# Optimization experiments

Measured on AMD Instinct MI355X. Metric: run time of the kernel, lower is better.

The kernel has to match this reference:

```python
import jax, jax.numpy as jnp
import numpy as np
from itertools import combinations

# ---- G(3,0,1) projective geometric algebra tables (blade order: grades 0..4, lexicographic) ----

def _build_tables():
    blades = [c for g in range(5) for c in combinations(range(4), g)]
    index = {b: i for i, b in enumerate(blades)}
    def mul(a, b, e0_sq):
        lst = list(a) + list(b)
        sign = 1
        for i in range(len(lst)):
            for j in range(len(lst) - 1 - i):
                if lst[j] > lst[j + 1]:
                    lst[j], lst[j + 1] = lst[j + 1], lst[j]
                    sign = -sign
        out, i = [], 0
        while i < len(lst):
            if i + 1 < len(lst) and lst[i] == lst[i + 1]:
                if lst[i] == 0:
                    sign *= e0_sq  # e0^2 = 0 in PGA geometric product
                i += 2
            else:
                out.append(lst[i]); i += 1
        return tuple(out), sign
    GP = np.zeros((16, 16, 16), np.float32)
    WEDGE = np.zeros((16, 16, 16), np.float32)
    for a in blades:
        for b in blades:
            bl, s = mul(a, b, 0)
            if s != 0:
                GP[index[a], index[b], index[bl]] += s
            if not (set(a) & set(b)):
                bl, s = mul(a, b, 1)
                WEDGE[index[a], index[b], index[bl]] += s
    D = np.zeros((16, 16), np.float32)
    for a in blades:
        c = tuple(sorted(set(range(4)) - set(a)))
        bl, s = mul(a, c, 1)  # e_a ^ e_c = s * e0123
        D[index[c], index[a]] = s
    Dinv = np.linalg.inv(D).astype(np.float32)
    # 9 Pin(3,0,1)-equivariant linear basis maps: 5 grade projections + 4 left-mult by e0
    B = np.zeros((9, 16, 16), np.float32)
    for i, a in enumerate(blades):
        B[len(a), i, i] = 1.0
        if 0 not in a:
            tgt = tuple(sorted((0,) + a))
            B[5 + len(a), index[tgt], i] = 1.0
    inner_idx = np.array([i for i, a in enumerate(blades) if 0 not in a])  # invariant inner product skips e0 blades
    return (jnp.asarray(GP), jnp.asarray(WEDGE), jnp.asarray(D), jnp.asarray(Dinv), jnp.asarray(B), jnp.asarray(inner_idx))

GP_T, WEDGE_T, DUAL, DUAL_INV, BASIS, INNER_IDX = _build_tables()
N_HEADS = 8  # gatr SelfAttentionConfig default


def equi_linear(x, W):
    # x: [..., in_ch, 16], W: [out_ch, in_ch, 9] -> [..., out_ch, 16]
    return jnp.einsum('...ik,oib,bjk->...oj', x, W, BASIS)


def equi_norm(x, eps=1e-6):
    sq = jnp.sum(jnp.take(x, INNER_IDX, axis=-1) ** 2, axis=-1)      # [..., C]
    factor = jnp.mean(sq, axis=-1, keepdims=True)[..., None]          # [..., 1, 1]
    return x * jax.lax.rsqrt(factor + eps)


def geometric_product(x, y):
    return jnp.einsum('...i,...j,ijk->...k', x, y, GP_T)


def equi_join(x, y):
    xd = jnp.einsum('ji,...i->...j', DUAL, x)
    yd = jnp.einsum('ji,...i->...j', DUAL, y)
    w = jnp.einsum('...i,...j,ijk->...k', xd, yd, WEDGE_T)
    return jnp.einsum('ji,...i->...j', DUAL_INV, w)


def attention(x, Wq, Wk, Wv, Wo):
    Bb, N, C, _ = x.shape
    ch = C // N_HEADS
    def split(h):
        return h.reshape(Bb, N, N_HEADS, ch, 16).transpose(0, 2, 1, 3, 4)  # [B,H,N,ch,16]
    q = split(equi_linear(x, Wq))
    k = split(equi_linear(x, Wk))
    v = split(equi_linear(x, Wv))
    qi = jnp.take(q, INNER_IDX, axis=-1)
    ki = jnp.take(k, INNER_IDX, axis=-1)
    logits = jnp.einsum('bhnck,bhmck->bhnm', qi, ki) / np.float32(np.sqrt(8 * ch))
    att = jax.nn.softmax(logits, axis=-1)
    out = jnp.einsum('bhnm,bhmck->bhnck', att, v)
    out = out.transpose(0, 2, 1, 3, 4).reshape(Bb, N, C, 16)
    return equi_linear(out, Wo)


def geo_mlp(x, Wl, Wr, Wm):
    C = x.shape[-2]
    half = C // 2
    left = equi_linear(x, Wl)
    right = equi_linear(x, Wr)
    gp = geometric_product(left[..., :half, :], right[..., :half, :])
    jn = equi_join(left[..., half:, :], right[..., half:, :])
    h = jnp.concatenate([gp, jn], axis=-2)
    h = h * jax.nn.gelu(h[..., 0:1], approximate=False)  # scalar-gated GELU
    return equi_linear(h, Wm)


def embed_point(p):
    # PGA point: homogeneous trivector, e123 coefficient 1
    z = jnp.zeros(p.shape[:-1] + (16,), p.dtype)
    z = z.at[..., 11].set(p[..., 2])
    z = z.at[..., 12].set(-p[..., 1])
    z = z.at[..., 13].set(p[..., 0])
    z = z.at[..., 14].set(1.0)
    return z


def reference(points, W_in, Wq, Wk, Wv, Wo, Wl, Wr, Wm, W_out):
    x = embed_point(points)[..., None, :]   # [B, N, 1, 16]
    x = equi_linear(x, W_in)                # [B, N, C, 16]
    def block(xc, p):
        wq, wk, wv, wo, wl, wr, wm = p
        xc = xc + attention(equi_norm(xc), wq, wk, wv, wo)
        xc = xc + geo_mlp(equi_norm(xc), wl, wr, wm)
        return xc, None
    x, _ = jax.lax.scan(block, x, (Wq, Wk, Wv, Wo, Wl, Wr, Wm))
    out = equi_linear(x, W_out)             # [B, N, 1, 16]
    return jnp.mean(out[..., 0], axis=(1, 2))  # [B]


def setup_inputs():
    key = jax.random.key(0)
    ks = jax.random.split(key, 12)
    B, N, C, L = 1, 2048, 16, 10
    def w(k, o, i):
        return jax.random.normal(k, (o, i, 9), jnp.float32) / np.float32(np.sqrt(9.0 * i))
    def wl(k, o, i):
        return jax.random.normal(k, (L, o, i, 9), jnp.float32) / np.float32(np.sqrt(9.0 * i))
    return {
        'points': jax.random.normal(ks[0], (B, N, 3), jnp.float32),
        'W_in': w(ks[1], C, 1),
        'Wq': wl(ks[2], C, C), 'Wk': wl(ks[3], C, C), 'Wv': wl(ks[4], C, C),
        'Wo': wl(ks[5], C, C), 'Wl': wl(ks[6], C, C), 'Wr': wl(ks[7], C, C),
        'Wm': wl(ks[8], C, C), 'W_out': w(ks[9], 1, C),
    }
```

## Files before the change

kernel.cpp:

```cpp
#include <hip/hip_runtime.h>
#include <math.h>

#define NTOK 2048

typedef short short8v __attribute__((ext_vector_type(8)));
typedef short short4v __attribute__((ext_vector_type(4)));
typedef float f32x4 __attribute__((ext_vector_type(4)));

__device__ __forceinline__ unsigned short f2bf(float x){
  unsigned u = __float_as_uint(x);
  u += 0x7fff + ((u>>16)&1);
  return (unsigned short)(u>>16);
}

struct GEnt { unsigned char i, j, k; signed char s; };

constexpr int IDX2MASK[16] = {0,1,2,4,8,3,5,9,6,10,12,7,11,13,14,15};
constexpr int MASK2IDX[16] = {0,1,2,5,3,6,8,11,4,7,9,12,10,13,14,15};

constexpr int rsign(int a, int b){
  int cnt=0;
  for(int i=0;i<4;++i) if((b>>i)&1) for(int j=i+1;j<4;++j) if((a>>j)&1) cnt++;
  return (cnt&1)?-1:1;
}

struct GPTab { GEnt e[192]; };
constexpr GPTab make_gp(){
  GPTab t{}; int n=0;
  for(int ia=0; ia<16; ++ia) for(int ib=0; ib<16; ++ib){
    int a=IDX2MASK[ia], b=IDX2MASK[ib];
    if(a&b&1) continue;
    t.e[n].i=(unsigned char)ia; t.e[n].j=(unsigned char)ib;
    t.e[n].k=(unsigned char)MASK2IDX[a^b]; t.e[n].s=(signed char)rsign(a,b);
    ++n;
  }
  return t;
}
static constexpr GPTab GP_TAB = make_gp();

struct JTab { GEnt e[81]; };
constexpr JTab make_join(){
  JTab t{}; int n=0;
  for(int ia=0; ia<16; ++ia) for(int ib=0; ib<16; ++ib){
    int a=IDX2MASK[ia], b=IDX2MASK[ib];
    if((a|b)!=15) continue;
    int ca=(~a)&15, cb=(~b)&15, k=a&b, ck=(~k)&15;
    int s = rsign(a,ca)*rsign(b,cb)*rsign(ca,cb)*rsign(k,ck);
    t.e[n].i=(unsigned char)ia; t.e[n].j=(unsigned char)ib;
    t.e[n].k=(unsigned char)MASK2IDX[k]; t.e[n].s=(signed char)s;
    ++n;
  }
  return t;
}
static constexpr JTab J_TAB = make_join();

constexpr int INNER[8] = {0,2,3,4,8,9,10,14};

__device__ __forceinline__ void apply_gp(float* o, const float* a, const float* b){
#pragma unroll
  for(int n=0;n<192;++n){
    const float s = (float)GP_TAB.e[n].s;
    o[GP_TAB.e[n].k] = fmaf(s*a[GP_TAB.e[n].i], b[GP_TAB.e[n].j], o[GP_TAB.e[n].k]);
  }
}
__device__ __forceinline__ void apply_join(float* o, const float* a, const float* b){
#pragma unroll
  for(int n=0;n<81;++n){
    const float s = (float)J_TAB.e[n].s;
    o[J_TAB.e[n].k] = fmaf(s*a[J_TAB.e[n].i], b[J_TAB.e[n].j], o[J_TAB.e[n].k]);
  }
}

__device__ __forceinline__ void elin_row(float acc[16], const float* xin, const float* w0p){
#pragma unroll
  for(int j=0;j<16;++j) acc[j]=0.0f;
#pragma unroll
  for(int i=0;i<16;++i){
    const float* w = w0p + i*9;
    const float4* xp = (const float4*)(xin + i*16);
    float4 A=xp[0], B=xp[1], Cc=xp[2], D=xp[3];
    float w0=w[0],w1=w[1],w2=w[2],w3=w[3],w4=w[4],w5=w[5],w6=w[6],w7=w[7],w8=w[8];
    acc[0] = fmaf(w0, A.x,  acc[0]);
    acc[1] = fmaf(w1, A.y,  acc[1]);
    acc[2] = fmaf(w1, A.z,  acc[2]);
    acc[3] = fmaf(w1, A.w,  acc[3]);
    acc[4] = fmaf(w1, B.x,  acc[4]);
    acc[5] = fmaf(w2, B.y,  acc[5]);
    acc[6] = fmaf(w2, B.z,  acc[6]);
    acc[7] = fmaf(w2, B.w,  acc[7]);
    acc[8] = fmaf(w2, Cc.x, acc[8]);
    acc[9] = fmaf(w2, Cc.y, acc[9]);
    acc[10]= fmaf(w2, Cc.z, acc[10]);
    acc[11]= fmaf(w3, Cc.w, acc[11]);
    acc[12]= fmaf(w3, D.x,  acc[12]);
    acc[13]= fmaf(w3, D.y,  acc[13]);
    acc[14]= fmaf(w3, D.z,  acc[14]);
    acc[15]= fmaf(w4, D.w,  acc[15]);
    acc[1] = fmaf(w5, A.x,  acc[1]);
    acc[5] = fmaf(w6, A.z,  acc[5]);
    acc[6] = fmaf(w6, A.w,  acc[6]);
    acc[7] = fmaf(w6, B.x,  acc[7]);
    acc[11]= fmaf(w7, Cc.x, acc[11]);
    acc[12]= fmaf(w7, Cc.y, acc[12]);
    acc[13]= fmaf(w7, Cc.z, acc[13]);
    acc[15]= fmaf(w8, D.z,  acc[15]);
  }
}

__device__ __forceinline__ float gelu_exact(float x){
  return 0.5f*x*(1.0f+erff(x*0.70710678118654752f));
}

#define WPAD 145
#define TBS  264
#define TPB  8

template<int MODE>
__global__ __launch_bounds__(128) void token_kernel(
    const float* __restrict__ points, const float* __restrict__ Win,
    const float* __restrict__ Wo, const float* __restrict__ Wl,
    const float* __restrict__ Wr, const float* __restrict__ Wm,
    const float* __restrict__ Wq, const float* __restrict__ Wk,
    const float* __restrict__ Wv, const float* __restrict__ Wout,
    const float* __restrict__ ATT, float* __restrict__ X,
    unsigned short* __restrict__ Qg16, unsigned short* __restrict__ Kg16,
    unsigned short* __restrict__ VgT, float* __restrict__ toksum)
{
  __shared__ float wlds[6*16*WPAD];
  __shared__ float buf[TPB*TBS];
  __shared__ float sred[TPB*16];
  const int tid = threadIdx.x;
  const int t = tid>>4, o = tid&15;
  const int n = blockIdx.x*TPB + t;

  auto stage = [&](float* dst, const float* src){
#pragma unroll
    for(int r=0;r<18;++r){
      int k = tid + r*128;
      dst[(k/144)*WPAD + (k%144)] = src[k];
    }
  };
  if (MODE==0){ stage(wlds+3*16*WPAD, Wq); stage(wlds+4*16*WPAD, Wk); stage(wlds+5*16*WPAD, Wv); }
  if (MODE==1){ stage(wlds+0*16*WPAD, Wl); stage(wlds+1*16*WPAD, Wr); stage(wlds+2*16*WPAD, Wm);
                stage(wlds+3*16*WPAD, Wq); stage(wlds+4*16*WPAD, Wk); stage(wlds+5*16*WPAD, Wv); }
  if (MODE==2){ stage(wlds+0*16*WPAD, Wl); stage(wlds+1*16*WPAD, Wr); stage(wlds+2*16*WPAD, Wm); }

  float* tb = buf + t*TBS;
  float xr[16];

  if (MODE==0){
    float px = points[n*3+0], py = points[n*3+1], pz = points[n*3+2];
    float w3 = Win[o*9+3], w8 = Win[o*9+8];
#pragma unroll
    for(int j=0;j<16;++j) xr[j]=0.0f;
    xr[11]= w3*pz; xr[12]= -w3*py; xr[13]= w3*px; xr[14]= w3; xr[15]= w8;
    float4* xg = (float4*)(X + (size_t)n*256 + o*16);
    xg[0]=make_float4(xr[0],xr[1],xr[2],xr[3]);
    xg[1]=make_float4(xr[4],xr[5],xr[6],xr[7]);
    xg[2]=make_float4(xr[8],xr[9],xr[10],xr[11]);
    xg[3]=make_float4(xr[12],xr[13],xr[14],xr[15]);
  } else {
    const float4* xg = (const float4*)(X + (size_t)n*256 + o*16);
    float4 a=xg[0],b=xg[1],c=xg[2],d=xg[3];
    xr[0]=a.x; xr[1]=a.y; xr[2]=a.z; xr[3]=a.w;
    xr[4]=b.x; xr[5]=b.y; xr[6]=b.z; xr[7]=b.w;
    xr[8]=c.x; xr[9]=c.y; xr[10]=c.z; xr[11]=c.w;
    xr[12]=d.x; xr[13]=d.y; xr[14]=d.z; xr[15]=d.w;
    const float4* ag = (const float4*)(ATT + (size_t)n*256 + o*16);
    float4* bp = (float4*)(tb + o*16);
    bp[0]=ag[0]; bp[1]=ag[1]; bp[2]=ag[2]; bp[3]=ag[3];
    __syncthreads();
    float acc[16];
    elin_row(acc, tb, Wo + o*144);
#pragma unroll
    for(int j=0;j<16;++j) xr[j]+=acc[j];
    float s=0;
#pragma unroll
    for(int z=0;z<8;++z){ float v=xr[INNER[z]]; s=fmaf(v,v,s); }
    sred[tid]=s; __syncthreads();
    float tot=0;
#pragma unroll
    for(int c2=0;c2<16;++c2) tot += sred[t*16+c2];
    float f = 1.0f/sqrtf(tot*(1.0f/16.0f)+1e-6f);
    float4* bp2=(float4*)(tb+o*16);
    bp2[0]=make_float4(xr[0]*f,xr[1]*f,xr[2]*f,xr[3]*f);
    bp2[1]=make_float4(xr[4]*f,xr[5]*f,xr[6]*f,xr[7]*f);
    bp2[2]=make_float4(xr[8]*f,xr[9]*f,xr[10]*f,xr[11]*f);
    bp2[3]=make_float4(xr[12]*f,xr[13]*f,xr[14]*f,xr[15]*f);
    __syncthreads();
    float L[16], R[16];
    elin_row(L, tb, wlds+0*16*WPAD + o*WPAD);
    elin_row(R, tb, wlds+1*16*WPAD + o*WPAD);
    float h[16];
#pragma unroll
    for(int j=0;j<16;++j) h[j]=0.0f;
    if (o<8) apply_gp(h,L,R); else apply_join(h,L,R);
    float gel = gelu_exact(h[0]);
#pragma unroll
    for(int j=0;j<16;++j) h[j]*=gel;
    __syncthreads();
    float4* bp3=(float4*)(tb+o*16);
    bp3[0]=make_float4(h[0],h[1],h[2],h[3]);
    bp3[1]=make_float4(h[4],h[5],h[6],h[7]);
    bp3[2]=make_float4(h[8],h[9],h[10],h[11]);
    bp3[3]=make_float4(h[12],h[13],h[14],h[15]);
    __syncthreads();
    float mm2[16];
    elin_row(mm2, tb, wlds+2*16*WPAD + o*WPAD);
#pragma unroll
    for(int j=0;j<16;++j) xr[j]+=mm2[j];
    if (MODE==1){
      float4* xs = (float4*)(X + (size_t)n*256 + o*16);
      xs[0]=make_float4(xr[0],xr[1],xr[2],xr[3]);
      xs[1]=make_float4(xr[4],xr[5],xr[6],xr[7]);
      xs[2]=make_float4(xr[8],xr[9],xr[10],xr[11]);
      xs[3]=make_float4(xr[12],xr[13],xr[14],xr[15]);
    }
  }

  if (MODE==2){
    sred[tid] = Wout[o*9]*xr[0];
    __syncthreads();
    if (o==0){
      float s2=0;
#pragma unroll
      for(int c2=0;c2<16;++c2) s2+=sred[t*16+c2];
      toksum[n]=s2;
    }
    return;
  }

  {
    float s=0;
#pragma unroll
    for(int z=0;z<8;++z){ float v=xr[INNER[z]]; s=fmaf(v,v,s); }
    sred[tid]=s; __syncthreads();
    float tot=0;
#pragma unroll
    for(int c2=0;c2<16;++c2) tot += sred[t*16+c2];
    float f2 = 1.0f/sqrtf(tot*(1.0f/16.0f)+1e-6f);
    float4* bp4=(float4*)(tb+o*16);
    bp4[0]=make_float4(xr[0]*f2,xr[1]*f2,xr[2]*f2,xr[3]*f2);
    bp4[1]=make_float4(xr[4]*f2,xr[5]*f2,xr[6]*f2,xr[7]*f2);
    bp4[2]=make_float4(xr[8]*f2,xr[9]*f2,xr[10]*f2,xr[11]*f2);
    bp4[3]=make_float4(xr[12]*f2,xr[13]*f2,xr[14]*f2,xr[15]*f2);
    __syncthreads();
    float q_[16],k_[16],v_[16];
    elin_row(q_, tb, wlds+3*16*WPAD+o*WPAD);
    elin_row(k_, tb, wlds+4*16*WPAD+o*WPAD);
    elin_row(v_, tb, wlds+5*16*WPAD+o*WPAD);
    int hh=o>>1, cc=o&1;
    {
      unsigned qw[4], kw[4];
#pragma unroll
      for(int j=0;j<4;++j){
        unsigned short a0=f2bf(q_[INNER[2*j]]*0.25f), a1=f2bf(q_[INNER[2*j+1]]*0.25f);
        unsigned short b0=f2bf(k_[INNER[2*j]]),       b1=f2bf(k_[INNER[2*j+1]]);
        qw[j] = (unsigned)a0 | ((unsigned)a1<<16);
        kw[j] = (unsigned)b0 | ((unsigned)b1<<16);
      }
      size_t rb = ((size_t)hh*NTOK + n)*16 + cc*8;
      *(uint4*)(Qg16 + rb) = make_uint4(qw[0],qw[1],qw[2],qw[3]);
      *(uint4*)(Kg16 + rb) = make_uint4(kw[0],kw[1],kw[2],kw[3]);
    }
    __syncthreads();
    {
      float4* vb = (float4*)(tb + o*16);
      vb[0]=make_float4(v_[0],v_[1],v_[2],v_[3]);
      vb[1]=make_float4(v_[4],v_[5],v_[6],v_[7]);
      vb[2]=make_float4(v_[8],v_[9],v_[10],v_[11]);
      vb[3]=make_float4(v_[12],v_[13],v_[14],v_[15]);
    }
    __syncthreads();
#pragma unroll
    for(int pp=0;pp<2;++pp){
      int p  = tid + pp*128;
      int h2 = p>>5, v2 = p&31;
      int oc = 2*h2 + (v2>>4), c2 = v2&15;
      unsigned vw[4];
#pragma unroll
      for(int j=0;j<4;++j){
        unsigned short e0=f2bf(buf[(2*j  )*TBS + oc*16 + c2]);
        unsigned short e1=f2bf(buf[(2*j+1)*TBS + oc*16 + c2]);
        vw[j]=(unsigned)e0 | ((unsigned)e1<<16);
      }
      *(uint4*)(VgT + ((size_t)(h2*32+v2))*NTOK + (size_t)blockIdx.x*TPB) = make_uint4(vw[0],vw[1],vw[2],vw[3]);
    }
  }
}

__global__ __launch_bounds__(256) void attn_kernel(
    const unsigned short* __restrict__ Qg16, const unsigned short* __restrict__ Kg16,
    const unsigned short* __restrict__ VgT,  float* __restrict__ ATT)
{
  __shared__ unsigned short Pl[4][2][16*36];
  __shared__ float cmb[4*32*17];
  __shared__ float ml[4*16*2];
  const int tid = threadIdx.x;
  const int l   = tid & 63, w = tid >> 6;
  const int h   = blockIdx.x >> 7, qb = blockIdx.x & 127;
  const int l15 = l & 15, lg = l >> 4;

  const short4v z4 = {0,0,0,0};
  short8v qa;
  {
    const short4v* qp = (const short4v*)(Qg16 + ((size_t)(h*NTOK + qb*16 + l15))*16 + lg*4);
    qa = __builtin_shufflevector(*qp, z4, 0,1,2,3,4,5,6,7);
  }

  f32x4 acc0 = {0,0,0,0}, acc1 = {0,0,0,0};
  float m[4]  = {-INFINITY,-INFINITY,-INFINITY,-INFINITY};
  float ls[4] = {0,0,0,0};
  const int key0 = w*512;

#pragma unroll 1
  for(int kc=0; kc<512; kc+=32){
    f32x4 S[2];
#pragma unroll
    for(int t2=0;t2<2;++t2){
      const short4v* kp = (const short4v*)(Kg16 + ((size_t)(h*NTOK + key0 + kc + t2*16 + l15))*16 + lg*4);
      short8v kf = __builtin_shufflevector(*kp, z4, 0,1,2,3,4,5,6,7);
      f32x4 z = {0,0,0,0};
      S[t2] = __builtin_amdgcn_mfma_f32_16x16x32_bf16(qa, kf, z, 0,0,0);
    }
    float corr[4];
#pragma unroll
    for(int r=0;r<4;++r){
      float mx = fmaxf(S[0][r], S[1][r]);
      mx = fmaxf(mx, __shfl_xor(mx, 1));
      mx = fmaxf(mx, __shfl_xor(mx, 2));
      mx = fmaxf(mx, __shfl_xor(mx, 4));
      mx = fmaxf(mx, __shfl_xor(mx, 8));
      float nm = fmaxf(m[r], mx);
      corr[r] = __expf(m[r] - nm);
      m[r] = nm;
    }
    float p0[4], p1[4];
#pragma unroll
    for(int r=0;r<4;++r){ p0[r] = __expf(S[0][r]-m[r]); p1[r] = __expf(S[1][r]-m[r]); }
#pragma unroll
    for(int r=0;r<4;++r){
      float s = p0[r] + p1[r];
      s += __shfl_xor(s, 1); s += __shfl_xor(s, 2);
      s += __shfl_xor(s, 4); s += __shfl_xor(s, 8);
      ls[r] = ls[r]*corr[r] + s;
      acc0[r] *= corr[r]; acc1[r] *= corr[r];
    }
    unsigned short* Pc = &Pl[w][(kc>>5)&1][0];
#pragma unroll
    for(int r=0;r<4;++r){
      Pc[(lg*4+r)*36 +      l15] = f2bf(p0[r]);
      Pc[(lg*4+r)*36 + 16 + l15] = f2bf(p1[r]);
    }
    asm volatile("s_waitcnt lgkmcnt(0)" ::: "memory");
    __builtin_amdgcn_sched_barrier(0);
    const short4v* pr0 = (const short4v*)(Pc + l15*36 +      lg*4);
    const short4v* pr1 = (const short4v*)(Pc + l15*36 + 16 + lg*4);
    short8v pa = __builtin_shufflevector(*pr0, *pr1, 0,1,2,3,4,5,6,7);
    size_t vbase = ((size_t)(h*32 + l15))*NTOK + key0 + kc;
    const short4v* vr0a = (const short4v*)(VgT + vbase + lg*4);
    const short4v* vr0b = (const short4v*)(VgT + vbase + 16 + lg*4);
    short8v vb0 = __builtin_shufflevector(*vr0a, *vr0b, 0,1,2,3,4,5,6,7);
    size_t vbase1 = vbase + (size_t)16*NTOK;
    const short4v* vr1a = (const short4v*)(VgT + vbase1 + lg*4);
    const short4v* vr1b = (const short4v*)(VgT + vbase1 + 16 + lg*4);
    short8v vb1 = __builtin_shufflevector(*vr1a, *vr1b, 0,1,2,3,4,5,6,7);
    acc0 = __builtin_amdgcn_mfma_f32_16x16x32_bf16(pa, vb0, acc0, 0,0,0);
    acc1 = __builtin_amdgcn_mfma_f32_16x16x32_bf16(pa, vb1, acc1, 0,0,0);
  }

  {
    float* cw = cmb + w*544;
#pragma unroll
    for(int r=0;r<4;++r){
      cw[ l15     *17 + lg*4 + r] = acc0[r];
      cw[(l15+16) *17 + lg*4 + r] = acc1[r];
    }
    if (l15 == 0){
#pragma unroll
      for(int r=0;r<4;++r){
        ml[(w*16 + lg*4 + r)*2]   = m[r];
        ml[(w*16 + lg*4 + r)*2+1] = ls[r];
      }
    }
  }
  __syncthreads();
  {
    int q = tid & 15, v = tid >> 4;
    float M = -INFINITY;
#pragma unroll
    for(int w2=0; w2<4; ++w2) M = fmaxf(M, ml[(w2*16+q)*2]);
    float L=0, a0=0, a1=0;
#pragma unroll
    for(int w2=0; w2<4; ++w2){
      float ww = __expf(ml[(w2*16+q)*2] - M);
      L  = fmaf(ml[(w2*16+q)*2+1], ww, L);
      a0 = fmaf(cmb[w2*544 +  v     *17 + q], ww, a0);
      a1 = fmaf(cmb[w2*544 + (v+16) *17 + q], ww, a1);
    }
    float inv = 1.0f/L;
    int n = qb*16 + q;
    ATT[(size_t)n*256 + (size_t)(2*h  )*16 + v] = a0*inv;
    ATT[(size_t)n*256 + (size_t)(2*h+1)*16 + v] = a1*inv;
  }
}

__global__ __launch_bounds__(256) void reduce_kernel(const float* __restrict__ tok, float* __restrict__ out){
  int tid=threadIdx.x;
  float s=0;
  for(int i=tid;i<NTOK;i+=256) s+=tok[i];
#pragma unroll
  for(int off=32;off>0;off>>=1) s += __shfl_down(s,off);
  __shared__ float red[4];
  if((tid&63)==0) red[tid>>6]=s;
  __syncthreads();
  if(tid==0) out[0]=(red[0]+red[1]+red[2]+red[3])*(1.0f/2048.0f);
}

extern "C" void kernel_launch(void* const* d_in, const int* in_sizes, int n_in,
                              void* d_out, int out_size, void* d_ws, size_t ws_size,
                              hipStream_t stream){
  const float* points=(const float*)d_in[0];
  const float* Win=(const float*)d_in[1];
  const float* Wq=(const float*)d_in[2];
  const float* Wk=(const float*)d_in[3];
  const float* Wv=(const float*)d_in[4];
  const float* Wo=(const float*)d_in[5];
  const float* Wl=(const float*)d_in[6];
  const float* Wr=(const float*)d_in[7];
  const float* Wm=(const float*)d_in[8];
  const float* Wout=(const float*)d_in[9];
  float* ws=(float*)d_ws;
  float* X    = ws;
  float* ATT  = ws + 524288;
  unsigned short* Qg16 = (unsigned short*)(ws + 1048576);
  unsigned short* Kg16 = (unsigned short*)(ws + 1179648);
  unsigned short* VgT  = (unsigned short*)(ws + 1310720);
  float* tok  = ws + 1572864;
  float* out=(float*)d_out;

  token_kernel<0><<<256,128,0,stream>>>(points,Win,nullptr,nullptr,nullptr,nullptr,
                                        Wq,Wk,Wv,nullptr,nullptr,X,Qg16,Kg16,VgT,nullptr);
  for(int l=0;l<10;++l){
    attn_kernel<<<1024,256,0,stream>>>(Qg16,Kg16,VgT,ATT);
    if(l<9){
      token_kernel<1><<<256,128,0,stream>>>(nullptr,nullptr,
          Wo+l*2304,Wl+l*2304,Wr+l*2304,Wm+l*2304,
          Wq+(l+1)*2304,Wk+(l+1)*2304,Wv+(l+1)*2304,nullptr,
          ATT,X,Qg16,Kg16,VgT,nullptr);
    } else {
      token_kernel<2><<<256,128,0,stream>>>(nullptr,nullptr,
          Wo+l*2304,Wl+l*2304,Wr+l*2304,Wm+l*2304,
          nullptr,nullptr,nullptr,Wout,
          ATT,X,nullptr,nullptr,nullptr,tok);
    }
  }
  reduce_kernel<<<1,256,0,stream>>>(tok,out);
}
```

Measured before the change: 692.5 us.

## Compute transposed scores so softmax probabilities stay in registers for PV MFMA

New measurement: 664.4 us. 1.04x faster.

```diff
diff --git a/kernel.cpp b/kernel.cpp
--- a/kernel.cpp
+++ b/kernel.cpp
@@ -1,4 +1,5 @@
 #include <hip/hip_runtime.h>
+#include <hip/hip_bf16.h>
 #include <math.h>
 
 #define NTOK 2048
@@ -6,11 +7,16 @@
 typedef short short8v __attribute__((ext_vector_type(8)));
 typedef short short4v __attribute__((ext_vector_type(4)));
 typedef float f32x4 __attribute__((ext_vector_type(4)));
+typedef unsigned u32x4 __attribute__((ext_vector_type(4)));
 
 __device__ __forceinline__ unsigned short f2bf(float x){
   unsigned u = __float_as_uint(x);
   u += 0x7fff + ((u>>16)&1);
   return (unsigned short)(u>>16);
+}
+__device__ __forceinline__ unsigned pack_bf2(float a, float b){
+  __hip_bfloat162 h = __float22bfloat162_rn(float2{a,b});
+  return *reinterpret_cast<unsigned*>(&h);
 }
 
 struct GEnt { unsigned char i, j, k; signed char s; };
@@ -293,7 +299,6 @@
     const unsigned short* __restrict__ Qg16, const unsigned short* __restrict__ Kg16,
     const unsigned short* __restrict__ VgT,  float* __restrict__ ATT)
 {
-  __shared__ unsigned short Pl[4][2][16*36];
   __shared__ float cmb[4*32*17];
   __shared__ float ml[4*16*2];
   const int tid = threadIdx.x;
@@ -302,71 +307,77 @@
   const int l15 = l & 15, lg = l >> 4;
 
   const short4v z4 = {0,0,0,0};
-  short8v qa;
+  short8v qf;
   {
     const short4v* qp = (const short4v*)(Qg16 + ((size_t)(h*NTOK + qb*16 + l15))*16 + lg*4);
-    qa = __builtin_shufflevector(*qp, z4, 0,1,2,3,4,5,6,7);
+    qf = __builtin_shufflevector(*qp, z4, 0,1,2,3,4,5,6,7);
   }
 
   f32x4 acc0 = {0,0,0,0}, acc1 = {0,0,0,0};
-  float m[4]  = {-INFINITY,-INFINITY,-INFINITY,-INFINITY};
-  float ls[4] = {0,0,0,0};
+  float m = -INFINITY, ls = 0.0f;
   const int key0 = w*512;
-
-#pragma unroll 1
-  for(int kc=0; kc<512; kc+=32){
-    f32x4 S[2];
-#pragma unroll
-    for(int t2=0;t2<2;++t2){
+  const size_t vrow = ((size_t)(h*32 + l15))*NTOK;
+
+#pragma unroll 2
+  for(int kc=0; kc<512; kc+=64){
+    f32x4 S[4];
+#pragma unroll
+    for(int t2=0;t2<4;++t2){
       const short4v* kp = (const short4v*)(Kg16 + ((size_t)(h*NTOK + key0 + kc + t2*16 + l15))*16 + lg*4);
       short8v kf = __builtin_shufflevector(*kp, z4, 0,1,2,3,4,5,6,7);
       f32x4 z = {0,0,0,0};
-      S[t2] = __builtin_amdgcn_mfma_f32_16x16x32_bf16(qa, kf, z, 0,0,0);
-    }
-    float corr[4];
-#pragma unroll
-    for(int r=0;r<4;++r){
-      float mx = fmaxf(S[0][r], S[1][r]);
-      mx = fmaxf(mx, __shfl_xor(mx, 1));
-      mx = fmaxf(mx, __shfl_xor(mx, 2));
-      mx = fmaxf(mx, __shfl_xor(mx, 4));
-      mx = fmaxf(mx, __shfl_xor(mx, 8));
-      float nm = fmaxf(m[r], mx);
-      corr[r] = __expf(m[r] - nm);
-      m[r] = nm;
-    }
-    float p0[4], p1[4];
-#pragma unroll
-    for(int r=0;r<4;++r){ p0[r] = __expf(S[0][r]-m[r]); p1[r] = __expf(S[1][r]-m[r]); }
-#pragma unroll
-    for(int r=0;r<4;++r){
-      float s = p0[r] + p1[r];
-      s += __shfl_xor(s, 1); s += __shfl_xor(s, 2);
-      s += __shfl_xor(s, 4); s += __shfl_xor(s, 8);
-      ls[r] = ls[r]*corr[r] + s;
-      acc0[r] *= corr[r]; acc1[r] *= corr[r];
-    }
-    unsigned short* Pc = &Pl[w][(kc>>5)&1][0];
-#pragma unroll
-    for(int r=0;r<4;++r){
-      Pc[(lg*4+r)*36 +      l15] = f2bf(p0[r]);
-      Pc[(lg*4+r)*36 + 16 + l15] = f2bf(p1[r]);
-    }
-    asm volatile("s_waitcnt lgkmcnt(0)" ::: "memory");
-    __builtin_amdgcn_sched_barrier(0);
-    const short4v* pr0 = (const short4v*)(Pc + l15*36 +      lg*4);
-    const short4v* pr1 = (const short4v*)(Pc + l15*36 + 16 + lg*4);
-    short8v pa = __builtin_shufflevector(*pr0, *pr1, 0,1,2,3,4,5,6,7);
-    size_t vbase = ((size_t)(h*32 + l15))*NTOK + key0 + kc;
-    const short4v* vr0a = (const short4v*)(VgT + vbase + lg*4);
-    const short4v* vr0b = (const short4v*)(VgT + vbase + 16 + lg*4);
-    short8v vb0 = __builtin_shufflevector(*vr0a, *vr0b, 0,1,2,3,4,5,6,7);
-    size_t vbase1 = vbase + (size_t)16*NTOK;
-    const short4v* vr1a = (const short4v*)(VgT + vbase1 + lg*4);
-    const short4v* vr1b = (const short4v*)(VgT + vbase1 + 16 + lg*4);
-    short8v vb1 = __builtin_shufflevector(*vr1a, *vr1b, 0,1,2,3,4,5,6,7);
-    acc0 = __builtin_amdgcn_mfma_f32_16x16x32_bf16(pa, vb0, acc0, 0,0,0);
-    acc1 = __builtin_amdgcn_mfma_f32_16x16x32_bf16(pa, vb1, acc1, 0,0,0);
+      S[t2] = __builtin_amdgcn_mfma_f32_16x16x32_bf16(kf, qf, z, 0,0,0);
+    }
+    float mx = S[0][0];
+#pragma unroll
+    for(int t2=0;t2<4;++t2)
+#pragma unroll
+      for(int r=0;r<4;++r) mx = fmaxf(mx, S[t2][r]);
+    mx = fmaxf(mx, __shfl_xor(mx, 16));
+    mx = fmaxf(mx, __shfl_xor(mx, 32));
+    float nm = fmaxf(m, mx);
+    float corr = __expf(m - nm);
+    m = nm;
+    float p[4][4];
+    float s = 0.0f;
+#pragma unroll
+    for(int t2=0;t2<4;++t2)
+#pragma unroll
+      for(int r=0;r<4;++r){ float pv = __expf(S[t2][r]-nm); p[t2][r]=pv; s += pv; }
+    s += __shfl_xor(s, 16);
+    s += __shfl_xor(s, 32);
+    ls = ls*corr + s;
+    float c0 = __shfl(corr, lg*4+0);
+    float c1 = __shfl(corr, lg*4+1);
+    float c2 = __shfl(corr, lg*4+2);
+    float c3 = __shfl(corr, lg*4+3);
+    acc0[0]*=c0; acc0[1]*=c1; acc0[2]*=c2; acc0[3]*=c3;
+    acc1[0]*=c0; acc1[1]*=c1; acc1[2]*=c2; acc1[3]*=c3;
+    u32x4 paw, paw2;
+    paw[0]=pack_bf2(p[0][0],p[0][1]); paw[1]=pack_bf2(p[0][2],p[0][3]);
+    paw[2]=pack_bf2(p[1][0],p[1][1]); paw[3]=pack_bf2(p[1][2],p[1][3]);
+    paw2[0]=pack_bf2(p[2][0],p[2][1]); paw2[1]=pack_bf2(p[2][2],p[2][3]);
+    paw2[2]=pack_bf2(p[3][0],p[3][1]); paw2[3]=pack_bf2(p[3][2],p[3][3]);
+    short8v pa  = *reinterpret_cast<short8v*>(&paw);
+    short8v pa2 = *reinterpret_cast<short8v*>(&paw2);
+    size_t vb = vrow + key0 + kc;
+    const short4v* v0a = (const short4v*)(VgT + vb + lg*4);
+    const short4v* v0b = (const short4v*)(VgT + vb + 16 + lg*4);
+    const short4v* v0c = (const short4v*)(VgT + vb + 32 + lg*4);
+    const short4v* v0d = (const short4v*)(VgT + vb + 48 + lg*4);
+    short8v vb0  = __builtin_shufflevector(*v0a, *v0b, 0,1,2,3,4,5,6,7);
+    short8v vb0b = __builtin_shufflevector(*v0c, *v0d, 0,1,2,3,4,5,6,7);
+    size_t vb1s = vb + (size_t)16*NTOK;
+    const short4v* v1a = (const short4v*)(VgT + vb1s + lg*4);
+    const short4v* v1b = (const short4v*)(VgT + vb1s + 16 + lg*4);
+    const short4v* v1c = (const short4v*)(VgT + vb1s + 32 + lg*4);
+    const short4v* v1d = (const short4v*)(VgT + vb1s + 48 + lg*4);
+    short8v vb1  = __builtin_shufflevector(*v1a, *v1b, 0,1,2,3,4,5,6,7);
+    short8v vb1b = __builtin_shufflevector(*v1c, *v1d, 0,1,2,3,4,5,6,7);
+    acc0 = __builtin_amdgcn_mfma_f32_16x16x32_bf16(pa,  vb0,  acc0, 0,0,0);
+    acc0 = __builtin_amdgcn_mfma_f32_16x16x32_bf16(pa2, vb0b, acc0, 0,0,0);
+    acc1 = __builtin_amdgcn_mfma_f32_16x16x32_bf16(pa,  vb1,  acc1, 0,0,0);
+    acc1 = __builtin_amdgcn_mfma_f32_16x16x32_bf16(pa2, vb1b, acc1, 0,0,0);
   }
 
   {
@@ -376,12 +387,9 @@
       cw[ l15     *17 + lg*4 + r] = acc0[r];
       cw[(l15+16) *17 + lg*4 + r] = acc1[r];
     }
-    if (l15 == 0){
-#pragma unroll
-      for(int r=0;r<4;++r){
-        ml[(w*16 + lg*4 + r)*2]   = m[r];
-        ml[(w*16 + lg*4 + r)*2+1] = ls[r];
-      }
+    if (lg == 0){
+      ml[(w*16 + l15)*2]   = m;
+      ml[(w*16 + l15)*2+1] = ls;
     }
   }
   __syncthreads();
```
